# Performance work log

Hardware: AMD Instinct MI355X
Metric: run time of the kernel (lower is better)

The kernel has to match this reference:

```python
import jax, jax.numpy as jnp
import numpy as np

N = 4194304  # number of sampled points (flattened)
W = 32       # hidden width
IN_PTS, IN_VIEWS = 3, 3


def setup_inputs() -> dict:
    key = jax.random.key(0)
    ks = jax.random.split(key, 13)
    def lin(k, fan_in, fan_out):
        # torch nn.Linear default init: U(-1/sqrt(fan_in), 1/sqrt(fan_in))
        bound = 1.0 / np.sqrt(fan_in)
        kw, kb = jax.random.split(k)
        w = jax.random.uniform(kw, (fan_in, fan_out), jnp.float32, -bound, bound)
        b = jax.random.uniform(kb, (fan_out,), jnp.float32, -bound, bound)
        return w, b
    x = jax.random.normal(ks[0], (N, IN_PTS + IN_VIEWS), jnp.float32)
    w0, b0 = lin(ks[1], IN_PTS, W)          # pts_linears[0]
    w1, b1 = lin(ks[2], W, W)               # pts_linears[1]
    wf, bf = lin(ks[3], W, W)               # feature_linear
    ws, bs = lin(ks[4], W, 1)               # sigma_linear
    wv, bv = lin(ks[5], IN_VIEWS + W, W)    # view_linears[0]
    wr, br = lin(ks[6], W, 3)               # rgb_linear
    return {"x": x, "w0": w0, "b0": b0, "w1": w1, "b1": b1,
            "wf": wf, "bf": bf, "ws": ws, "bs": bs,
            "wv": wv, "bv": bv, "wr": wr, "br": br}


def reference(x, w0, b0, w1, b1, wf, bf, ws, bs, wv, bv, wr, br):
    pts, views = x[..., :IN_PTS], x[..., IN_PTS:]
    h = jax.nn.relu(pts @ w0 + b0)
    h = jax.nn.relu(h @ w1 + b1)
    sigma = h @ ws + bs                     # [N, 1]
    feature = h @ wf + bf                   # [N, W]
    h = jnp.concatenate([feature, views], axis=-1)  # [N, W+3]
    h = jax.nn.relu(h @ wv + bv)
    rgb = h @ wr + br                       # [N, 3]
    return jnp.concatenate([rgb, sigma], axis=-1)   # [N, 4]
```

## Files before the change

kernel.cpp:

```cpp
#include <hip/hip_runtime.h>


#define NPTS   4194304
#define NTILES (NPTS / 16)

typedef _Float16 f16;
typedef _Float16 f16x2 __attribute__((ext_vector_type(2)));
typedef _Float16 f16x8 __attribute__((ext_vector_type(8)));
typedef float    f32x4 __attribute__((ext_vector_type(4)));

union H8 { f16x8 v; unsigned u[4]; };

static __device__ __forceinline__ unsigned pkrtz(float a, float b) {
    return __builtin_bit_cast(unsigned, __builtin_amdgcn_cvt_pkrtz(a, b));
}
static __device__ __forceinline__ unsigned relu2(unsigned w) {
    f16x2 h = __builtin_bit_cast(f16x2, w);
    f16x2 z = (f16x2)(f16)0.f;
    return __builtin_bit_cast(unsigned, __builtin_elementwise_max(h, z));
}

#define MFMA(A, B, C) __builtin_amdgcn_mfma_f32_16x16x32_f16((A), (B), (C), 0, 0, 0)

__global__ __launch_bounds__(256, 5) void kilonerf_r10(
    const float* __restrict__ x,
    const float* __restrict__ w0, const float* __restrict__ b0,
    const float* __restrict__ w1, const float* __restrict__ b1,
    const float* __restrict__ wf, const float* __restrict__ bf,
    const float* __restrict__ ws, const float* __restrict__ bs,
    const float* __restrict__ wv, const float* __restrict__ bv,
    const float* __restrict__ wr, const float* __restrict__ br,
    float* __restrict__ out)
{
    const int lane = threadIdx.x & 63;
    const int g = lane >> 4;
    const int c = lane & 15;

    int kk[8];
#pragma unroll
    for (int j = 0; j < 8; ++j) kk[j] = (j < 4) ? (4 * g + j) : (16 + 4 * g + (j - 4));

    f16x8 aw0[2], aw1[2], awf[2], awv[2], awv2[2], aws, awr;
#pragma unroll
    for (int t = 0; t < 2; ++t) {
#pragma unroll
        for (int j = 0; j < 8; ++j) {
            const int m = c + 16 * t;
            const int k = kk[j];
            aw0[t][j]  = (k < 3) ? (f16)w0[k * 32 + m]
                        : (k == 3 ? (f16)b0[m] : (f16)0.f);
            aw1[t][j]  = (f16)w1[k * 32 + m];
            awf[t][j]  = (f16)wf[k * 32 + m];
            awv[t][j]  = (f16)wv[k * 32 + m];
            awv2[t][j] = (k >= 16 && k < 19) ? (f16)wv[(32 + (k - 16)) * 32 + m]
                        : (k == 19 ? (f16)bv[m] : (f16)0.f);
        }
    }
#pragma unroll
    for (int j = 0; j < 8; ++j) {
        aws[j] = (c == 0) ? (f16)ws[kk[j]] : (f16)0.f;
        awr[j] = (c < 3) ? (f16)wr[kk[j] * 3 + c] : (f16)0.f;
    }

    f32x4 b1f[2], bff[2];
#pragma unroll
    for (int t = 0; t < 2; ++t)
#pragma unroll
        for (int r = 0; r < 4; ++r) {
            const int m = 4 * g + r + 16 * t;
            b1f[t][r] = b1[m];
            bff[t][r] = bf[m];
        }

    const float br0 = br[0], br1 = br[1], br2 = br[2], bs0 = bs[0];

    const f32x4 zf = {0.f, 0.f, 0.f, 0.f};

    const int wslot  = blockIdx.x * 4 + (threadIdx.x >> 6);
    const int nslots = gridDim.x * 4;

    for (int tile = wslot; tile < NTILES; tile += nslots) {
        const float2* xp2 = reinterpret_cast<const float2*>(
            x + (size_t)(tile * 16 + c) * 6);
        const float2 a0 = xp2[0], a1 = xp2[1], a2 = xp2[2];
        H8 bx;
        bx.u[0] = pkrtz(a0.x, a0.y);
        bx.u[1] = pkrtz(a1.x, 1.0f);
        bx.u[2] = pkrtz(a1.y, a2.x);
        bx.u[3] = pkrtz(a2.y, 1.0f);

        f32x4 c00 = MFMA(aw0[0], bx.v, zf);
        f32x4 c01 = MFMA(aw0[1], bx.v, zf);
        f32x4 cv0 = MFMA(awv2[0], bx.v, zf);
        f32x4 cv1 = MFMA(awv2[1], bx.v, zf);

        H8 bh0;
        bh0.u[0] = relu2(pkrtz(c00[0], c00[1]));
        bh0.u[1] = relu2(pkrtz(c00[2], c00[3]));
        bh0.u[2] = relu2(pkrtz(c01[0], c01[1]));
        bh0.u[3] = relu2(pkrtz(c01[2], c01[3]));

        f32x4 c10 = MFMA(aw1[0], bh0.v, b1f[0]);
        f32x4 c11 = MFMA(aw1[1], bh0.v, b1f[1]);
        H8 bh1;
        bh1.u[0] = relu2(pkrtz(c10[0], c10[1]));
        bh1.u[1] = relu2(pkrtz(c10[2], c10[3]));
        bh1.u[2] = relu2(pkrtz(c11[0], c11[1]));
        bh1.u[3] = relu2(pkrtz(c11[2], c11[3]));

        f32x4 cs = MFMA(aws, bh1.v, zf);

        f32x4 cf0 = MFMA(awf[0], bh1.v, bff[0]);
        f32x4 cf1 = MFMA(awf[1], bh1.v, bff[1]);
        H8 bft;
        bft.u[0] = pkrtz(cf0[0], cf0[1]);
        bft.u[1] = pkrtz(cf0[2], cf0[3]);
        bft.u[2] = pkrtz(cf1[0], cf1[1]);
        bft.u[3] = pkrtz(cf1[2], cf1[3]);

        cv0 = MFMA(awv[0], bft.v, cv0);
        cv1 = MFMA(awv[1], bft.v, cv1);
        H8 bhv;
        bhv.u[0] = relu2(pkrtz(cv0[0], cv0[1]));
        bhv.u[1] = relu2(pkrtz(cv0[2], cv0[3]));
        bhv.u[2] = relu2(pkrtz(cv1[0], cv1[1]));
        bhv.u[3] = relu2(pkrtz(cv1[2], cv1[3]));

        f32x4 cr = MFMA(awr, bhv.v, zf);

        if (g == 0) {
            float4 o = make_float4(cr[0] + br0, cr[1] + br1,
                                   cr[2] + br2, cs[0] + bs0);
            *reinterpret_cast<float4*>(out + (size_t)(tile * 16 + c) * 4) = o;
        }
    }
}

extern "C" void kernel_launch(void* const* d_in, const int* in_sizes, int n_in,
                              void* d_out, int out_size, void* d_ws, size_t ws_size,
                              hipStream_t stream) {
    const float* x  = (const float*)d_in[0];
    const float* w0 = (const float*)d_in[1];
    const float* b0 = (const float*)d_in[2];
    const float* w1 = (const float*)d_in[3];
    const float* b1 = (const float*)d_in[4];
    const float* wf = (const float*)d_in[5];
    const float* bf = (const float*)d_in[6];
    const float* ws = (const float*)d_in[7];
    const float* bs = (const float*)d_in[8];
    const float* wv = (const float*)d_in[9];
    const float* bv = (const float*)d_in[10];
    const float* wr = (const float*)d_in[11];
    const float* br = (const float*)d_in[12];
    float* out = (float*)d_out;

    dim3 block(256);
    dim3 grid(2048);
    kilonerf_r10<<<grid, block, 0, stream>>>(x, w0, b0, w1, b1, wf, bf,
                                             ws, bs, wv, bv, wr, br, out);
}
```

Measured before the change: 63.03 us.

## Switch MLP to 32x32x16 MFMA tiles with folded feature bias and scalar sigma

Each wave now processes 32 points per tile using the 32x32x16 f16 MFMA, with the K=32 layers split into two accumulating K=16 halves. The feature bias is folded into the view-layer bias via a precomputed wv^T·bf term. Sigma is computed with per-lane FMAs plus a cross-half shuffle instead of a mostly-empty MFMA. The aim is fewer MFMA issues and less padding waste per point. The cost is larger accumulator register use, so the occupancy hint drops from 5 to 4 waves.

Result: no change. 62.66 us (-0.6%).

```diff
diff --git a/kernel.cpp b/kernel.cpp
--- a/kernel.cpp
+++ b/kernel.cpp
@@ -2,12 +2,12 @@
 
 
 #define NPTS   4194304
-#define NTILES (NPTS / 16)
+#define NT32   (NPTS / 32)
 
 typedef _Float16 f16;
 typedef _Float16 f16x2 __attribute__((ext_vector_type(2)));
 typedef _Float16 f16x8 __attribute__((ext_vector_type(8)));
-typedef float    f32x4 __attribute__((ext_vector_type(4)));
+typedef float    f32x16 __attribute__((ext_vector_type(16)));
 
 union H8 { f16x8 v; unsigned u[4]; };
 
@@ -20,9 +20,9 @@
     return __builtin_bit_cast(unsigned, __builtin_elementwise_max(h, z));
 }
 
-#define MFMA(A, B, C) __builtin_amdgcn_mfma_f32_16x16x32_f16((A), (B), (C), 0, 0, 0)
+#define MFMA32(A, B, C) __builtin_amdgcn_mfma_f32_32x32x16_f16((A), (B), (C), 0, 0, 0)
 
-__global__ __launch_bounds__(256, 5) void kilonerf_r10(
+__global__ __launch_bounds__(256, 4) void kilonerf_m32(
     const float* __restrict__ x,
     const float* __restrict__ w0, const float* __restrict__ b0,
     const float* __restrict__ w1, const float* __restrict__ b1,
@@ -33,105 +33,135 @@
     float* __restrict__ out)
 {
     const int lane = threadIdx.x & 63;
-    const int g = lane >> 4;
-    const int c = lane & 15;
+    const int m  = lane & 31;
+    const int hi = lane >> 5;
 
-    int kk[8];
+    int sj[8], row[16];
 #pragma unroll
-    for (int j = 0; j < 8; ++j) kk[j] = (j < 4) ? (4 * g + j) : (16 + 4 * g + (j - 4));
+    for (int j = 0; j < 8; ++j)  sj[j]  = (j & 3) + 8 * (j >> 2) + 4 * hi;
+#pragma unroll
+    for (int r = 0; r < 16; ++r) row[r] = (r & 3) + 8 * (r >> 2) + 4 * hi;
 
-    f16x8 aw0[2], aw1[2], awf[2], awv[2], awv2[2], aws, awr;
-#pragma unroll
-    for (int t = 0; t < 2; ++t) {
-#pragma unroll
-        for (int j = 0; j < 8; ++j) {
-            const int m = c + 16 * t;
-            const int k = kk[j];
-            aw0[t][j]  = (k < 3) ? (f16)w0[k * 32 + m]
-                        : (k == 3 ? (f16)b0[m] : (f16)0.f);
-            aw1[t][j]  = (f16)w1[k * 32 + m];
-            awf[t][j]  = (f16)wf[k * 32 + m];
-            awv[t][j]  = (f16)wv[k * 32 + m];
-            awv2[t][j] = (k >= 16 && k < 19) ? (f16)wv[(32 + (k - 16)) * 32 + m]
-                        : (k == 19 ? (f16)bv[m] : (f16)0.f);
-        }
-    }
+    float bve = bv[m];
+#pragma unroll 8
+    for (int k = 0; k < 32; ++k) bve = fmaf(wv[k * 32 + m], bf[k], bve);
+
+    f16x8 aw0x, awv2x, aw1lo, aw1hi, awflo, awfhi, awvlo, awvhi, awrlo, awrhi;
 #pragma unroll
     for (int j = 0; j < 8; ++j) {
-        aws[j] = (c == 0) ? (f16)ws[kk[j]] : (f16)0.f;
-        awr[j] = (c < 3) ? (f16)wr[kk[j] * 3 + c] : (f16)0.f;
+        const int k = sj[j];
+        aw0x[j]  = (k < 3) ? (f16)w0[k * 32 + m]
+                  : (k == 3 ? (f16)b0[m] : (f16)0.f);
+        awv2x[j] = (k >= 4 && k < 7) ? (f16)wv[(32 + (k - 4)) * 32 + m]
+                  : (k == 7 ? (f16)bve : (f16)0.f);
+        aw1lo[j] = (f16)w1[k * 32 + m];
+        aw1hi[j] = (f16)w1[(16 + k) * 32 + m];
+        awflo[j] = (f16)wf[k * 32 + m];
+        awfhi[j] = (f16)wf[(16 + k) * 32 + m];
+        awvlo[j] = (f16)wv[k * 32 + m];
+        awvhi[j] = (f16)wv[(16 + k) * 32 + m];
+        awrlo[j] = (m < 3) ? (f16)wr[k * 3 + m] : (f16)0.f;
+        awrhi[j] = (m < 3) ? (f16)wr[(16 + k) * 3 + m] : (f16)0.f;
     }
 
-    f32x4 b1f[2], bff[2];
+    float wsv[16];
+    f32x16 b1c;
 #pragma unroll
-    for (int t = 0; t < 2; ++t)
-#pragma unroll
-        for (int r = 0; r < 4; ++r) {
-            const int m = 4 * g + r + 16 * t;
-            b1f[t][r] = b1[m];
-            bff[t][r] = bf[m];
-        }
+    for (int r = 0; r < 16; ++r) {
+        wsv[r] = ws[row[r]];
+        b1c[r] = b1[row[r]];
+    }
 
     const float br0 = br[0], br1 = br[1], br2 = br[2], bs0 = bs[0];
 
-    const f32x4 zf = {0.f, 0.f, 0.f, 0.f};
+    f32x16 zf;
+#pragma unroll
+    for (int r = 0; r < 16; ++r) zf[r] = 0.f;
 
     const int wslot  = blockIdx.x * 4 + (threadIdx.x >> 6);
     const int nslots = gridDim.x * 4;
 
-    for (int tile = wslot; tile < NTILES; tile += nslots) {
+    for (int tile = wslot; tile < NT32; tile += nslots) {
         const float2* xp2 = reinterpret_cast<const float2*>(
-            x + (size_t)(tile * 16 + c) * 6);
+            x + (size_t)(tile * 32 + m) * 6);
         const float2 a0 = xp2[0], a1 = xp2[1], a2 = xp2[2];
+
+        const float fa = hi ? a1.y : a0.x;
+        const float fb = hi ? a2.x : a0.y;
+        const float fc = hi ? a2.y : a1.x;
         H8 bx;
-        bx.u[0] = pkrtz(a0.x, a0.y);
-        bx.u[1] = pkrtz(a1.x, 1.0f);
-        bx.u[2] = pkrtz(a1.y, a2.x);
-        bx.u[3] = pkrtz(a2.y, 1.0f);
+        bx.u[0] = pkrtz(fa, fb);
+        bx.u[1] = pkrtz(fc, 1.0f);
+        bx.u[2] = 0u;
+        bx.u[3] = 0u;
 
-        f32x4 c00 = MFMA(aw0[0], bx.v, zf);
-        f32x4 c01 = MFMA(aw0[1], bx.v, zf);
-        f32x4 cv0 = MFMA(awv2[0], bx.v, zf);
-        f32x4 cv1 = MFMA(awv2[1], bx.v, zf);
+        f32x16 c0 = MFMA32(aw0x, bx.v, zf);
+        f32x16 cv = MFMA32(awv2x, bx.v, zf);
 
-        H8 bh0;
-        bh0.u[0] = relu2(pkrtz(c00[0], c00[1]));
-        bh0.u[1] = relu2(pkrtz(c00[2], c00[3]));
-        bh0.u[2] = relu2(pkrtz(c01[0], c01[1]));
-        bh0.u[3] = relu2(pkrtz(c01[2], c01[3]));
+        H8 blo, bhi;
+        blo.u[0] = relu2(pkrtz(c0[0], c0[1]));
+        blo.u[1] = relu2(pkrtz(c0[2], c0[3]));
+        blo.u[2] = relu2(pkrtz(c0[4], c0[5]));
+        blo.u[3] = relu2(pkrtz(c0[6], c0[7]));
+        bhi.u[0] = relu2(pkrtz(c0[8], c0[9]));
+        bhi.u[1] = relu2(pkrtz(c0[10], c0[11]));
+        bhi.u[2] = relu2(pkrtz(c0[12], c0[13]));
+        bhi.u[3] = relu2(pkrtz(c0[14], c0[15]));
 
-        f32x4 c10 = MFMA(aw1[0], bh0.v, b1f[0]);
-        f32x4 c11 = MFMA(aw1[1], bh0.v, b1f[1]);
-        H8 bh1;
-        bh1.u[0] = relu2(pkrtz(c10[0], c10[1]));
-        bh1.u[1] = relu2(pkrtz(c10[2], c10[3]));
-        bh1.u[2] = relu2(pkrtz(c11[0], c11[1]));
-        bh1.u[3] = relu2(pkrtz(c11[2], c11[3]));
+        f32x16 c1 = MFMA32(aw1lo, blo.v, b1c);
+        c1 = MFMA32(aw1hi, bhi.v, c1);
 
-        f32x4 cs = MFMA(aws, bh1.v, zf);
+        float s0 = 0.f, s1 = 0.f, s2 = 0.f, s3 = 0.f;
+#pragma unroll
+        for (int r = 0; r < 4; ++r) {
+            s0 = fmaf(fmaxf(c1[r],      0.f), wsv[r],      s0);
+            s1 = fmaf(fmaxf(c1[4 + r],  0.f), wsv[4 + r],  s1);
+            s2 = fmaf(fmaxf(c1[8 + r],  0.f), wsv[8 + r],  s2);
+            s3 = fmaf(fmaxf(c1[12 + r], 0.f), wsv[12 + r], s3);
+        }
+        float sg = (s0 + s1) + (s2 + s3);
+        sg += __shfl_xor(sg, 32);
 
-        f32x4 cf0 = MFMA(awf[0], bh1.v, bff[0]);
-        f32x4 cf1 = MFMA(awf[1], bh1.v, bff[1]);
-        H8 bft;
-        bft.u[0] = pkrtz(cf0[0], cf0[1]);
-        bft.u[1] = pkrtz(cf0[2], cf0[3]);
-        bft.u[2] = pkrtz(cf1[0], cf1[1]);
-        bft.u[3] = pkrtz(cf1[2], cf1[3]);
+        blo.u[0] = relu2(pkrtz(c1[0], c1[1]));
+        blo.u[1] = relu2(pkrtz(c1[2], c1[3]));
+        blo.u[2] = relu2(pkrtz(c1[4], c1[5]));
+        blo.u[3] = relu2(pkrtz(c1[6], c1[7]));
+        bhi.u[0] = relu2(pkrtz(c1[8], c1[9]));
+        bhi.u[1] = relu2(pkrtz(c1[10], c1[11]));
+        bhi.u[2] = relu2(pkrtz(c1[12], c1[13]));
+        bhi.u[3] = relu2(pkrtz(c1[14], c1[15]));
 
-        cv0 = MFMA(awv[0], bft.v, cv0);
-        cv1 = MFMA(awv[1], bft.v, cv1);
-        H8 bhv;
-        bhv.u[0] = relu2(pkrtz(cv0[0], cv0[1]));
-        bhv.u[1] = relu2(pkrtz(cv0[2], cv0[3]));
-        bhv.u[2] = relu2(pkrtz(cv1[0], cv1[1]));
-        bhv.u[3] = relu2(pkrtz(cv1[2], cv1[3]));
+        f32x16 cf = MFMA32(awflo, blo.v, zf);
+        cf = MFMA32(awfhi, bhi.v, cf);
 
-        f32x4 cr = MFMA(awr, bhv.v, zf);
+        blo.u[0] = pkrtz(cf[0], cf[1]);
+        blo.u[1] = pkrtz(cf[2], cf[3]);
+        blo.u[2] = pkrtz(cf[4], cf[5]);
+        blo.u[3] = pkrtz(cf[6], cf[7]);
+        bhi.u[0] = pkrtz(cf[8], cf[9]);
+        bhi.u[1] = pkrtz(cf[10], cf[11]);
+        bhi.u[2] = pkrtz(cf[12], cf[13]);
+        bhi.u[3] = pkrtz(cf[14], cf[15]);
 
-        if (g == 0) {
+        cv = MFMA32(awvlo, blo.v, cv);
+        cv = MFMA32(awvhi, bhi.v, cv);
+
+        blo.u[0] = relu2(pkrtz(cv[0], cv[1]));
+        blo.u[1] = relu2(pkrtz(cv[2], cv[3]));
+        blo.u[2] = relu2(pkrtz(cv[4], cv[5]));
+        blo.u[3] = relu2(pkrtz(cv[6], cv[7]));
+        bhi.u[0] = relu2(pkrtz(cv[8], cv[9]));
+        bhi.u[1] = relu2(pkrtz(cv[10], cv[11]));
+        bhi.u[2] = relu2(pkrtz(cv[12], cv[13]));
+        bhi.u[3] = relu2(pkrtz(cv[14], cv[15]));
+
+        f32x16 cr = MFMA32(awrlo, blo.v, zf);
+        cr = MFMA32(awrhi, bhi.v, cr);
+
+        if (hi == 0) {
             float4 o = make_float4(cr[0] + br0, cr[1] + br1,
-                                   cr[2] + br2, cs[0] + bs0);
-            *reinterpret_cast<float4*>(out + (size_t)(tile * 16 + c) * 4) = o;
+                                   cr[2] + br2, sg + bs0);
+            *reinterpret_cast<float4*>(out + (size_t)(tile * 32 + m) * 4) = o;
         }
     }
 }
@@ -156,6 +186,6 @@
 
     dim3 block(256);
     dim3 grid(2048);
-    kilonerf_r10<<<grid, block, 0, stream>>>(x, w0, b0, w1, b1, wf, bf,
+    kilonerf_m32<<<grid, block, 0, stream>>>(x, w0, b0, w1, b1, wf, bf,
                                              ws, bs, wv, bv, wr, br, out);
 }
```
